# Kernel optimization log

Hardware: AMD Instinct MI355X
Metric: run time of the kernel (lower is better)

Reference implementation:

```python
import jax, jax.numpy as jnp
import numpy as np

B, S = 4, 2048
N_EMBED = 1024
D_FF = 4 * N_EMBED
N_EXPERTS = 8
TOP_K = 2


def setup_inputs() -> dict:
    key = jax.random.key(0)
    ks = jax.random.split(key, 12)
    std = 0.02
    return {
        "x": jax.random.normal(ks[0], (B, S, N_EMBED), dtype=jnp.float32),
        "noise_u": jax.random.uniform(ks[1], (B, S, N_EXPERTS), dtype=jnp.float32),
        # router params
        "wg": jax.random.normal(ks[2], (N_EMBED, N_EXPERTS), dtype=jnp.float32) * std,
        "bg": jnp.zeros((N_EXPERTS,), dtype=jnp.float32),
        "wn": jax.random.normal(ks[3], (N_EMBED, N_EXPERTS), dtype=jnp.float32) * std,
        "bn": jnp.zeros((N_EXPERTS,), dtype=jnp.float32),
        # stacked expert params [E, ...]
        "w1": jax.random.normal(ks[4], (N_EXPERTS, N_EMBED, D_FF), dtype=jnp.float32) * std,
        "b1": jnp.zeros((N_EXPERTS, D_FF), dtype=jnp.float32),
        "w2": jax.random.normal(ks[5], (N_EXPERTS, D_FF, N_EMBED), dtype=jnp.float32) * std,
        "b2": jnp.zeros((N_EXPERTS, N_EMBED), dtype=jnp.float32),
    }


def reference(x, noise_u, wg, bg, wn, bn, w1, b1, w2, b2):
    # ---- NoisyTopKRouter ----
    logits = x @ wg + bg                              # [B,S,E]
    noise_logits = x @ wn + bn                        # [B,S,E]
    noisy = logits + noise_u * jax.nn.softplus(noise_logits)
    top_vals, top_idx = jax.lax.top_k(noisy, TOP_K)   # [B,S,K]
    # selected-expert mask; scatter of top-k logits == where(selected, noisy, -inf)
    sel = jax.nn.one_hot(top_idx, N_EXPERTS).sum(axis=-2) > 0   # [B,S,E] bool
    sparse_logits = jnp.where(sel, noisy, -jnp.inf)
    gates = jax.nn.softmax(sparse_logits, axis=-1)    # zero for unselected experts
    # ---- per-expert MLP, combined with gate weights (zero gate => no contribution) ----
    out = jnp.zeros_like(x)
    for e in range(N_EXPERTS):
        h = jax.nn.relu(x @ w1[e] + b1[e])            # [B,S,4d]
        y = h @ w2[e] + b2[e]                         # [B,S,d]
        out = out + gates[..., e:e + 1] * y
    return out
```

## Files before the change

kernel.cpp:

```cpp
#include <hip/hip_runtime.h>
#include <hip/hip_bf16.h>


#define T_TOK 8192
#define D_EMB 1024
#define DFF   4096
#define N_EXP 8
#define BM 128
#define BN 128
#define BK 64

typedef __attribute__((ext_vector_type(8))) short bf16x8;
typedef __attribute__((ext_vector_type(4))) float floatx4;
typedef unsigned short bf16_t;

__device__ __forceinline__ bf16_t f2bf(float f) {
  union { float f; unsigned u; } a; a.f = f;
  unsigned u = a.u;
  return (bf16_t)((u + 0x7fffu + ((u >> 16) & 1u)) >> 16);
}

__global__ __launch_bounds__(256) void cvt_x_k(const float* __restrict__ x,
                                               bf16_t* __restrict__ xb) {
  int i = (blockIdx.x * 256 + threadIdx.x) * 4;
  float4 v = *(const float4*)(x + i);
  ushort4 o;
  o.x = f2bf(v.x); o.y = f2bf(v.y); o.z = f2bf(v.z); o.w = f2bf(v.w);
  *(ushort4*)(xb + i) = o;
}

__global__ __launch_bounds__(256) void tcvt_k(const float* __restrict__ in,
                                              bf16_t* __restrict__ outp,
                                              int K, int N) {
  __shared__ float tile[32][33];
  int e  = blockIdx.z;
  int n0 = blockIdx.x * 32;
  int k0 = blockIdx.y * 32;
  int tx = threadIdx.x;
  int ty = threadIdx.y;
  const float* src = in + (size_t)e * K * N;
#pragma unroll
  for (int l = 0; l < 32; l += 8)
    tile[ty + l][tx] = src[(size_t)(k0 + ty + l) * N + (n0 + tx)];
  __syncthreads();
  bf16_t* dst = outp + (size_t)e * K * N;
#pragma unroll
  for (int l = 0; l < 32; l += 8)
    dst[(size_t)(n0 + ty + l) * K + (k0 + tx)] = f2bf(tile[tx][ty + l]);
}

__global__ __launch_bounds__(256) void router_k(
    const float* __restrict__ x, const float* __restrict__ nu,
    const float* __restrict__ wg, const float* __restrict__ bgp,
    const float* __restrict__ wn, const float* __restrict__ bnp,
    int* __restrict__ cnt, int* __restrict__ tok, float* __restrict__ gate) {
  int t = blockIdx.x;
  int tid = threadIdx.x;
  float gl[8] = {0,0,0,0,0,0,0,0};
  float nl[8] = {0,0,0,0,0,0,0,0};
  const float* xr = x + (size_t)t * D_EMB;
  for (int i = tid; i < D_EMB; i += 256) {
    float xv = xr[i];
    float4 a0 = *(const float4*)(wg + i * 8);
    float4 a1 = *(const float4*)(wg + i * 8 + 4);
    float4 c0 = *(const float4*)(wn + i * 8);
    float4 c1 = *(const float4*)(wn + i * 8 + 4);
    gl[0] += xv * a0.x; gl[1] += xv * a0.y; gl[2] += xv * a0.z; gl[3] += xv * a0.w;
    gl[4] += xv * a1.x; gl[5] += xv * a1.y; gl[6] += xv * a1.z; gl[7] += xv * a1.w;
    nl[0] += xv * c0.x; nl[1] += xv * c0.y; nl[2] += xv * c0.z; nl[3] += xv * c0.w;
    nl[4] += xv * c1.x; nl[5] += xv * c1.y; nl[6] += xv * c1.z; nl[7] += xv * c1.w;
  }
  __shared__ float red[4][16];
  int lane = tid & 63;
  int wv = tid >> 6;
#pragma unroll
  for (int o = 0; o < 16; ++o) {
    float v = (o < 8) ? gl[o] : nl[o - 8];
#pragma unroll
    for (int s = 32; s > 0; s >>= 1) v += __shfl_down(v, s, 64);
    if (lane == 0) red[wv][o] = v;
  }
  __syncthreads();
  if (tid == 0) {
    float noisy[8];
#pragma unroll
    for (int e = 0; e < 8; ++e) {
      float lg = red[0][e] + red[1][e] + red[2][e] + red[3][e] + bgp[e];
      float nz = red[0][8 + e] + red[1][8 + e] + red[2][8 + e] + red[3][8 + e] + bnp[e];
      float sp = fmaxf(nz, 0.f) + log1pf(expf(-fabsf(nz)));
      noisy[e] = lg + nu[(size_t)t * 8 + e] * sp;
    }
    int e1 = 0;
#pragma unroll
    for (int e = 1; e < 8; ++e) if (noisy[e] > noisy[e1]) e1 = e;
    int e2 = -1;
#pragma unroll
    for (int e = 0; e < 8; ++e) {
      if (e == e1) continue;
      if (e2 < 0 || noisy[e] > noisy[e2]) e2 = e;
    }
    float d = expf(noisy[e2] - noisy[e1]);
    float g1 = 1.f / (1.f + d);
    float g2 = d / (1.f + d);
    int p1 = atomicAdd(&cnt[e1], 1);
    tok[e1 * T_TOK + p1] = t; gate[e1 * T_TOK + p1] = g1;
    int p2 = atomicAdd(&cnt[e2], 1);
    tok[e2 * T_TOK + p2] = t; gate[e2 * T_TOK + p2] = g2;
  }
}

__global__ void scan_k(const int* __restrict__ cnt, int* __restrict__ offs) {
  if (threadIdx.x == 0 && blockIdx.x == 0) {
    int a = 0;
    for (int e = 0; e < N_EXP; ++e) { offs[e] = a; a += cnt[e]; }
    offs[N_EXP] = a;
  }
}

__global__ __launch_bounds__(256) void gemm1_k(
    const bf16_t* __restrict__ xb, const bf16_t* __restrict__ w1T,
    const float* __restrict__ b1p, const int* __restrict__ cnt,
    const int* __restrict__ offs, const int* __restrict__ tok,
    bf16_t* __restrict__ h) {
  const int NT = DFF / BN;
  const int MT = T_TOK / BM;
  int bid = blockIdx.x;
  int e = bid / (MT * NT);
  int rem = bid % (MT * NT);
  int mt = rem / NT;
  int nt = rem % NT;
  int cnte = cnt[e];
  if (mt * BM >= cnte) return;
  int rows = min(BM, cnte - mt * BM);

  __shared__ bf16_t As[BM][BK + 8];
  __shared__ bf16_t Bs[BN][BK + 8];
  __shared__ int stok[BM];

  int tid = threadIdx.x;
  if (tid < BM) {
    int r = mt * BM + ((tid < rows) ? tid : 0);
    stok[tid] = tok[e * T_TOK + r];
  }
  __syncthreads();

  int lane = tid & 63;
  int wv = tid >> 6;
  int m0 = (wv & 1) * 64;
  int n0 = (wv >> 1) * 64;
  int lm = lane & 15;
  int lq = lane >> 4;

  floatx4 acc[4][4];
#pragma unroll
  for (int i = 0; i < 4; ++i)
#pragma unroll
    for (int j = 0; j < 4; ++j)
#pragma unroll
      for (int r = 0; r < 4; ++r) acc[i][j][r] = 0.f;

  int srow = tid >> 1;
  int soff = (tid & 1) * 32;
  size_t arow = (size_t)stok[srow] * D_EMB + soff;
  const bf16_t* wbase = w1T + ((size_t)e * DFF + nt * BN + srow) * D_EMB + soff;

  for (int kk = 0; kk < D_EMB; kk += BK) {
    const uint4* ga = (const uint4*)(xb + arow + kk);
    const uint4* gb = (const uint4*)(wbase + kk);
    uint4 a0 = ga[0], a1 = ga[1], a2 = ga[2], a3 = ga[3];
    uint4 b0 = gb[0], b1v = gb[1], b2v = gb[2], b3v = gb[3];
    uint4* la = (uint4*)&As[srow][soff];
    uint4* lb = (uint4*)&Bs[srow][soff];
    la[0] = a0; la[1] = a1; la[2] = a2; la[3] = a3;
    lb[0] = b0; lb[1] = b1v; lb[2] = b2v; lb[3] = b3v;
    __syncthreads();
#pragma unroll
    for (int ks = 0; ks < BK; ks += 32) {
      bf16x8 af[4], bfr[4];
#pragma unroll
      for (int i = 0; i < 4; ++i)
        af[i] = *(const bf16x8*)&As[m0 + i * 16 + lm][ks + lq * 8];
#pragma unroll
      for (int j = 0; j < 4; ++j)
        bfr[j] = *(const bf16x8*)&Bs[n0 + j * 16 + lm][ks + lq * 8];
#pragma unroll
      for (int i = 0; i < 4; ++i)
#pragma unroll
        for (int j = 0; j < 4; ++j)
          acc[i][j] = __builtin_amdgcn_mfma_f32_16x16x32_bf16(af[i], bfr[j], acc[i][j], 0, 0, 0);
    }
    __syncthreads();
  }

  int hbase = offs[e] + mt * BM;
#pragma unroll
  for (int i = 0; i < 4; ++i) {
    int lr0 = m0 + i * 16 + lq * 4;
#pragma unroll
    for (int r = 0; r < 4; ++r) {
      if (lr0 + r < rows) {
        size_t hrow = (size_t)(hbase + lr0 + r) * DFF;
#pragma unroll
        for (int j = 0; j < 4; ++j) {
          int col = nt * BN + n0 + j * 16 + lm;
          float v = acc[i][j][r] + b1p[e * DFF + col];
          h[hrow + col] = f2bf(fmaxf(v, 0.f));
        }
      }
    }
  }
}

__global__ __launch_bounds__(256) void gemm2_k(
    const bf16_t* __restrict__ h, const bf16_t* __restrict__ w2T,
    const float* __restrict__ b2p, const int* __restrict__ cnt,
    const int* __restrict__ offs, const int* __restrict__ tok,
    const float* __restrict__ gate, float* __restrict__ out) {
  const int NT = D_EMB / BN;
  const int MT = T_TOK / BM;
  int bid = blockIdx.x;
  int e = bid / (MT * NT);
  int rem = bid % (MT * NT);
  int mt = rem / NT;
  int nt = rem % NT;
  int cnte = cnt[e];
  if (mt * BM >= cnte) return;
  int rows = min(BM, cnte - mt * BM);

  __shared__ bf16_t As[BM][BK + 8];
  __shared__ bf16_t Bs[BN][BK + 8];
  __shared__ int stok[BM];
  __shared__ float sgate[BM];

  int tid = threadIdx.x;
  if (tid < BM) {
    int idx = e * T_TOK + mt * BM + ((tid < rows) ? tid : 0);
    stok[tid] = tok[idx];
    sgate[tid] = gate[idx];
  }
  __syncthreads();

  int lane = tid & 63;
  int wv = tid >> 6;
  int m0 = (wv & 1) * 64;
  int n0 = (wv >> 1) * 64;
  int lm = lane & 15;
  int lq = lane >> 4;

  floatx4 acc[4][4];
#pragma unroll
  for (int i = 0; i < 4; ++i)
#pragma unroll
    for (int j = 0; j < 4; ++j)
#pragma unroll
      for (int r = 0; r < 4; ++r) acc[i][j][r] = 0.f;

  int srow = tid >> 1;
  int soff = (tid & 1) * 32;
  int srow_c = (srow < rows) ? srow : 0;
  const bf16_t* abase = h + ((size_t)(offs[e] + mt * BM + srow_c)) * DFF + soff;
  const bf16_t* wbase = w2T + ((size_t)e * D_EMB + nt * BN + srow) * DFF + soff;

  for (int kk = 0; kk < DFF; kk += BK) {
    const uint4* ga = (const uint4*)(abase + kk);
    const uint4* gb = (const uint4*)(wbase + kk);
    uint4 a0 = ga[0], a1 = ga[1], a2 = ga[2], a3 = ga[3];
    uint4 b0 = gb[0], b1v = gb[1], b2v = gb[2], b3v = gb[3];
    uint4* la = (uint4*)&As[srow][soff];
    uint4* lb = (uint4*)&Bs[srow][soff];
    la[0] = a0; la[1] = a1; la[2] = a2; la[3] = a3;
    lb[0] = b0; lb[1] = b1v; lb[2] = b2v; lb[3] = b3v;
    __syncthreads();
#pragma unroll
    for (int ks = 0; ks < BK; ks += 32) {
      bf16x8 af[4], bfr[4];
#pragma unroll
      for (int i = 0; i < 4; ++i)
        af[i] = *(const bf16x8*)&As[m0 + i * 16 + lm][ks + lq * 8];
#pragma unroll
      for (int j = 0; j < 4; ++j)
        bfr[j] = *(const bf16x8*)&Bs[n0 + j * 16 + lm][ks + lq * 8];
#pragma unroll
      for (int i = 0; i < 4; ++i)
#pragma unroll
        for (int j = 0; j < 4; ++j)
          acc[i][j] = __builtin_amdgcn_mfma_f32_16x16x32_bf16(af[i], bfr[j], acc[i][j], 0, 0, 0);
    }
    __syncthreads();
  }

#pragma unroll
  for (int i = 0; i < 4; ++i) {
    int lr0 = m0 + i * 16 + lq * 4;
#pragma unroll
    for (int r = 0; r < 4; ++r) {
      int lr = lr0 + r;
      if (lr < rows) {
        int t = stok[lr];
        float g = sgate[lr];
#pragma unroll
        for (int j = 0; j < 4; ++j) {
          int col = nt * BN + n0 + j * 16 + lm;
          float v = g * (acc[i][j][r] + b2p[e * D_EMB + col]);
          unsafeAtomicAdd(&out[(size_t)t * D_EMB + col], v);
        }
      }
    }
  }
}

extern "C" void kernel_launch(void* const* d_in, const int* in_sizes, int n_in,
                              void* d_out, int out_size, void* d_ws, size_t ws_size,
                              hipStream_t stream) {
  const float* x  = (const float*)d_in[0];
  const float* nu = (const float*)d_in[1];
  const float* wg = (const float*)d_in[2];
  const float* bg = (const float*)d_in[3];
  const float* wn = (const float*)d_in[4];
  const float* bn = (const float*)d_in[5];
  const float* w1 = (const float*)d_in[6];
  const float* b1 = (const float*)d_in[7];
  const float* w2 = (const float*)d_in[8];
  const float* b2 = (const float*)d_in[9];
  float* out = (float*)d_out;

  char* ws = (char*)d_ws;
  size_t o = 0;
  int* cnt  = (int*)(ws + o);
  int* offs = cnt + 8;
  o += 256;
  int*   tok  = (int*)(ws + o);   o += (size_t)N_EXP * T_TOK * 4;
  float* gate = (float*)(ws + o); o += (size_t)N_EXP * T_TOK * 4;
  bf16_t* xb  = (bf16_t*)(ws + o); o += (size_t)T_TOK * D_EMB * 2;
  bf16_t* w1T = (bf16_t*)(ws + o); o += (size_t)N_EXP * D_EMB * DFF * 2;
  bf16_t* w2T = (bf16_t*)(ws + o); o += (size_t)N_EXP * D_EMB * DFF * 2;
  bf16_t* h   = (bf16_t*)(ws + o); o += (size_t)2 * T_TOK * DFF * 2;
  (void)o; (void)ws_size; (void)in_sizes; (void)n_in;

  hipMemsetAsync(cnt, 0, 256, stream);
  hipMemsetAsync(out, 0, (size_t)out_size * sizeof(float), stream);

  cvt_x_k<<<(T_TOK * D_EMB) / 1024, 256, 0, stream>>>(x, xb);
  tcvt_k<<<dim3(DFF / 32, D_EMB / 32, N_EXP), dim3(32, 8), 0, stream>>>(w1, w1T, D_EMB, DFF);
  tcvt_k<<<dim3(D_EMB / 32, DFF / 32, N_EXP), dim3(32, 8), 0, stream>>>(w2, w2T, DFF, D_EMB);
  router_k<<<T_TOK, 256, 0, stream>>>(x, nu, wg, bg, wn, bn, cnt, tok, gate);
  scan_k<<<1, 64, 0, stream>>>(cnt, offs);
  gemm1_k<<<N_EXP * (T_TOK / BM) * (DFF / BN), 256, 0, stream>>>(xb, w1T, b1, cnt, offs, tok, h);
  gemm2_k<<<N_EXP * (T_TOK / BM) * (D_EMB / BN), 256, 0, stream>>>(h, w2T, b2, cnt, offs, tok, gate, out);
}
```

Before: 1.068 ms.

## Load GEMM tiles directly into LDS and interleave workgroups across experts

Both expert GEMM kernels now stage A and B tiles through global_load_lds (16-byte direct-to-LDS loads), which removes the register round trip and the separate LDS stores. The LDS tiles lose their padding, so fragment reads may hit more bank conflicts. Per-thread row pointers are precomputed, and the shared token-index staging in gemm1 is removed. Block IDs are also remapped so consecutive workgroups spread across the eight experts, which balances early-exit blocks and may change L2 reuse.

```diff
diff --git a/kernel.cpp b/kernel.cpp
--- a/kernel.cpp
+++ b/kernel.cpp
@@ -1,5 +1,4 @@
 #include <hip/hip_runtime.h>
-#include <hip/hip_bf16.h>
 
 
 #define T_TOK 8192
@@ -18,6 +17,12 @@
   union { float f; unsigned u; } a; a.f = f;
   unsigned u = a.u;
   return (bf16_t)((u + 0x7fffu + ((u >> 16) & 1u)) >> 16);
+}
+
+__device__ __forceinline__ void gl_lds16(const bf16_t* g, bf16_t* l) {
+  __builtin_amdgcn_global_load_lds(
+      (const __attribute__((address_space(1))) void*)g,
+      (__attribute__((address_space(3))) void*)l, 16, 0, 0);
 }
 
 __global__ __launch_bounds__(256) void cvt_x_k(const float* __restrict__ x,
@@ -124,7 +129,9 @@
     bf16_t* __restrict__ h) {
   const int NT = DFF / BN;
   const int MT = T_TOK / BM;
-  int bid = blockIdx.x;
+  const int NWG = N_EXP * MT * NT;
+  int b0 = blockIdx.x;
+  int bid = (b0 & 7) * (NWG >> 3) + (b0 >> 3);
   int e = bid / (MT * NT);
   int rem = bid % (MT * NT);
   int mt = rem / NT;
@@ -133,19 +140,24 @@
   if (mt * BM >= cnte) return;
   int rows = min(BM, cnte - mt * BM);
 
-  __shared__ bf16_t As[BM][BK + 8];
-  __shared__ bf16_t Bs[BN][BK + 8];
-  __shared__ int stok[BM];
+  __shared__ bf16_t As[BM * BK];
+  __shared__ bf16_t Bs[BN * BK];
 
   int tid = threadIdx.x;
-  if (tid < BM) {
-    int r = mt * BM + ((tid < rows) ? tid : 0);
-    stok[tid] = tok[e * T_TOK + r];
-  }
-  __syncthreads();
-
   int lane = tid & 63;
   int wv = tid >> 6;
+  int rq = tid >> 3, c8 = tid & 7;
+  const bf16_t* aptr[4];
+  const bf16_t* bptr[4];
+#pragma unroll
+  for (int i = 0; i < 4; ++i) {
+    int r = i * 32 + rq;
+    int rr = (r < rows) ? r : 0;
+    int t = tok[e * T_TOK + mt * BM + rr];
+    aptr[i] = xb + (size_t)t * D_EMB + c8 * 8;
+    bptr[i] = w1T + ((size_t)e * DFF + nt * BN + r) * D_EMB + c8 * 8;
+  }
+
   int m0 = (wv & 1) * 64;
   int n0 = (wv >> 1) * 64;
   int lm = lane & 15;
@@ -159,30 +171,22 @@
 #pragma unroll
       for (int r = 0; r < 4; ++r) acc[i][j][r] = 0.f;
 
-  int srow = tid >> 1;
-  int soff = (tid & 1) * 32;
-  size_t arow = (size_t)stok[srow] * D_EMB + soff;
-  const bf16_t* wbase = w1T + ((size_t)e * DFF + nt * BN + srow) * D_EMB + soff;
-
   for (int kk = 0; kk < D_EMB; kk += BK) {
-    const uint4* ga = (const uint4*)(xb + arow + kk);
-    const uint4* gb = (const uint4*)(wbase + kk);
-    uint4 a0 = ga[0], a1 = ga[1], a2 = ga[2], a3 = ga[3];
-    uint4 b0 = gb[0], b1v = gb[1], b2v = gb[2], b3v = gb[3];
-    uint4* la = (uint4*)&As[srow][soff];
-    uint4* lb = (uint4*)&Bs[srow][soff];
-    la[0] = a0; la[1] = a1; la[2] = a2; la[3] = a3;
-    lb[0] = b0; lb[1] = b1v; lb[2] = b2v; lb[3] = b3v;
+#pragma unroll
+    for (int i = 0; i < 4; ++i) {
+      gl_lds16(aptr[i] + kk, As + i * 2048 + wv * 512);
+      gl_lds16(bptr[i] + kk, Bs + i * 2048 + wv * 512);
+    }
     __syncthreads();
 #pragma unroll
     for (int ks = 0; ks < BK; ks += 32) {
       bf16x8 af[4], bfr[4];
 #pragma unroll
       for (int i = 0; i < 4; ++i)
-        af[i] = *(const bf16x8*)&As[m0 + i * 16 + lm][ks + lq * 8];
+        af[i] = *(const bf16x8*)&As[(m0 + i * 16 + lm) * BK + ks + lq * 8];
 #pragma unroll
       for (int j = 0; j < 4; ++j)
-        bfr[j] = *(const bf16x8*)&Bs[n0 + j * 16 + lm][ks + lq * 8];
+        bfr[j] = *(const bf16x8*)&Bs[(n0 + j * 16 + lm) * BK + ks + lq * 8];
 #pragma unroll
       for (int i = 0; i < 4; ++i)
 #pragma unroll
@@ -218,7 +222,9 @@
     const float* __restrict__ gate, float* __restrict__ out) {
   const int NT = D_EMB / BN;
   const int MT = T_TOK / BM;
-  int bid = blockIdx.x;
+  const int NWG = N_EXP * MT * NT;
+  int b0 = blockIdx.x;
+  int bid = (b0 & 7) * (NWG >> 3) + (b0 >> 3);
   int e = bid / (MT * NT);
   int rem = bid % (MT * NT);
   int mt = rem / NT;
@@ -227,8 +233,8 @@
   if (mt * BM >= cnte) return;
   int rows = min(BM, cnte - mt * BM);
 
-  __shared__ bf16_t As[BM][BK + 8];
-  __shared__ bf16_t Bs[BN][BK + 8];
+  __shared__ bf16_t As[BM * BK];
+  __shared__ bf16_t Bs[BN * BK];
   __shared__ int stok[BM];
   __shared__ float sgate[BM];
 
@@ -238,10 +244,20 @@
     stok[tid] = tok[idx];
     sgate[tid] = gate[idx];
   }
-  __syncthreads();
 
   int lane = tid & 63;
   int wv = tid >> 6;
+  int rq = tid >> 3, c8 = tid & 7;
+  const bf16_t* aptr[4];
+  const bf16_t* bptr[4];
+#pragma unroll
+  for (int i = 0; i < 4; ++i) {
+    int r = i * 32 + rq;
+    int rr = (r < rows) ? r : 0;
+    aptr[i] = h + (size_t)(offs[e] + mt * BM + rr) * DFF + c8 * 8;
+    bptr[i] = w2T + ((size_t)e * D_EMB + nt * BN + r) * DFF + c8 * 8;
+  }
+
   int m0 = (wv & 1) * 64;
   int n0 = (wv >> 1) * 64;
   int lm = lane & 15;
@@ -255,31 +271,22 @@
 #pragma unroll
       for (int r = 0; r < 4; ++r) acc[i][j][r] = 0.f;
 
-  int srow = tid >> 1;
-  int soff = (tid & 1) * 32;
-  int srow_c = (srow < rows) ? srow : 0;
-  const bf16_t* abase = h + ((size_t)(offs[e] + mt * BM + srow_c)) * DFF + soff;
-  const bf16_t* wbase = w2T + ((size_t)e * D_EMB + nt * BN + srow) * DFF + soff;
-
   for (int kk = 0; kk < DFF; kk += BK) {
-    const uint4* ga = (const uint4*)(abase + kk);
-    const uint4* gb = (const uint4*)(wbase + kk);
-    uint4 a0 = ga[0], a1 = ga[1], a2 = ga[2], a3 = ga[3];
-    uint4 b0 = gb[0], b1v = gb[1], b2v = gb[2], b3v = gb[3];
-    uint4* la = (uint4*)&As[srow][soff];
-    uint4* lb = (uint4*)&Bs[srow][soff];
-    la[0] = a0; la[1] = a1; la[2] = a2; la[3] = a3;
-    lb[0] = b0; lb[1] = b1v; lb[2] = b2v; lb[3] = b3v;
+#pragma unroll
+    for (int i = 0; i < 4; ++i) {
+      gl_lds16(aptr[i] + kk, As + i * 2048 + wv * 512);
+      gl_lds16(bptr[i] + kk, Bs + i * 2048 + wv * 512);
+    }
     __syncthreads();
 #pragma unroll
     for (int ks = 0; ks < BK; ks += 32) {
       bf16x8 af[4], bfr[4];
 #pragma unroll
       for (int i = 0; i < 4; ++i)
-        af[i] = *(const bf16x8*)&As[m0 + i * 16 + lm][ks + lq * 8];
+        af[i] = *(const bf16x8*)&As[(m0 + i * 16 + lm) * BK + ks + lq * 8];
 #pragma unroll
       for (int j = 0; j < 4; ++j)
-        bfr[j] = *(const bf16x8*)&Bs[n0 + j * 16 + lm][ks + lq * 8];
+        bfr[j] = *(const bf16x8*)&Bs[(n0 + j * 16 + lm) * BK + ks + lq * 8];
 #pragma unroll
       for (int i = 0; i < 4; ++i)
 #pragma unroll
```

Result: slower. 1.213 ms (+13.6%).
